# Performance work log

Measured on AMD Instinct MI355X. Metric: run time of the kernel, lower is better.

The kernel has to match this reference:

```python
import jax, jax.numpy as jnp
import numpy as np

B, N, D, E, F, K = 2, 2048, 768, 8, 3072, 2
V_MAX = 3.0
FEAT_CLAMP = 10.0


def setup_inputs() -> dict:
    key = jax.random.key(0)
    ks = jax.random.split(key, 8)
    s = lambda k, shape, sc: (jax.random.normal(k, shape, jnp.float32) * sc)
    return {
        "x": s(ks[0], (B, N, D), 1.0),
        "v_w": s(ks[1], (D,), 0.02),
        "v_b": jnp.zeros((), jnp.float32),
        "gate_w": s(ks[2], (D, E), 0.02),
        "gate_b": jnp.zeros((E,), jnp.float32),
        "w1": s(ks[3], (E, D, F), 0.02),
        "b1": jnp.zeros((E, F), jnp.float32),
        "w2": s(ks[4], (E, F, D), 0.02),
        "b2": jnp.zeros((E, D), jnp.float32),
        "out_w": s(ks[5], (2, D), 0.02),
        "out_b": jnp.zeros((D,), jnp.float32),
        "bk_scale": jnp.ones((D,), jnp.float32),
    }


def bk_green_diag(a):
    # a: (B, N) complex64 diagonal of (H_eps - z), unit off-diagonals.
    # Stable two-sided continued-fraction (Thomas/LDU) recursion:
    #   d_i = a_i - 1/d_{i-1},  e_i = a_i - 1/e_{i+1},  G_ii = 1/(d_i + e_i - a_i)
    aT = jnp.swapaxes(a, 0, 1)  # (N, B)

    def step(c, ai):
        d = ai - 1.0 / c
        return d, d

    d0 = aT[0]
    _, d_rest = jax.lax.scan(step, d0, aT[1:])
    d = jnp.concatenate([d0[None], d_rest], axis=0)  # (N, B)

    eN = aT[-1]
    _, e_rest = jax.lax.scan(step, eN, aT[:-1], reverse=True)
    e = jnp.concatenate([e_rest, eN[None]], axis=0)  # (N, B)

    G = 1.0 / (d + e - aT)
    return jnp.swapaxes(G, 0, 1)  # (B, N) complex


def reference(x, v_w, v_b, gate_w, gate_b, w1, b1, w2, b2, out_w, out_b, bk_scale):
    # --- potential projection: v = clamp(Linear(x), +-3) ---
    v = jnp.clip(x @ v_w + v_b, -V_MAX, V_MAX)  # (B, N)
    # H_eps diagonal = -2 + v, z = 1j  ->  A = H_eps - z
    a = ((-2.0 + v).astype(jnp.complex64) - 1j)
    G = bk_green_diag(a)  # (B, N) complex
    feats = jnp.stack([G.real, G.imag], axis=-1)  # (B, N, 2)

    # --- sparse MoE FFN (top-k softmax gating, GELU experts) ---
    logits = x @ gate_w + gate_b  # (B, N, E)
    probs = jax.nn.softmax(logits, axis=-1)
    topv, topi = jax.lax.top_k(probs, K)
    topv = topv / jnp.sum(topv, axis=-1, keepdims=True)
    comb = jnp.sum(topv[..., None] * jax.nn.one_hot(topi, E, dtype=x.dtype), axis=2)  # (B, N, E)
    h = jax.nn.gelu(jnp.einsum("bnd,edf->bnef", x, w1) + b1)  # (B, N, E, F)
    y = jnp.einsum("bnef,efd->bned", h, w2) + b2  # (B, N, E, D)
    ffn_out = jnp.einsum("bne,bned->bnd", comb, y)

    # --- spectral branch: clamp features, project to d_model, scale ---
    feats_c = jnp.clip(feats, -FEAT_CLAMP, FEAT_CLAMP)
    spec_out = feats_c @ out_w + out_b  # (B, N, D)
    return ffn_out + bk_scale * spec_out
```

## Files before the change

### kernel.cpp

```cpp
#include <hip/hip_runtime.h>
#include <hip/hip_bf16.h>

#define BB 2
#define NN 2048
#define DD 768
#define EE 8
#define FF 3072
#define TOK (BB*NN)
#define ROWS_CAP 9216
#define TILES 72

typedef __attribute__((ext_vector_type(8))) __bf16 bf16x8;
typedef __attribute__((ext_vector_type(4))) float floatx4;

#define OFF_CTRL    0ull
#define OFF_V       1024ull
#define OFF_TOKE    17408ull
#define OFF_TOKW    50176ull
#define OFF_ROWTOK  82944ull
#define OFF_ROWW    119808ull
#define OFF_SLOT    156672ull
#define OFF_FEATS   189440ull
#define OFF_W2T     222208ull
#define OFF_XBF     37970944ull
#define OFF_W1T     44262400ull
#define OFF_H       82011136ull
#define OFF_Y       OFF_XBF

__device__ __forceinline__ ushort f2b(float f) {
    union { float f; unsigned int i; } v; v.f = f;
    unsigned int u = v.i;
    unsigned int r = (u + 0x7FFFu + ((u >> 16) & 1u)) >> 16;
    return (ushort)r;
}
__device__ __forceinline__ unsigned int pk2(float lo, float hi) {
    union { float f; unsigned int u; } a, b;
    a.f = lo; b.f = hi;
    unsigned int ra = ((a.u + 0x7FFFu + ((a.u >> 16) & 1u)) >> 16) & 0xFFFFu;
    unsigned int rb = (b.u + 0x7FFFu + ((b.u >> 16) & 1u)) & 0xFFFF0000u;
    return ra | rb;
}
__device__ __forceinline__ float gelu_f(float x) {
    float z = 0.7978845608028654f * x * (1.f + 0.044715f * x * x);
    z = fminf(fmaxf(z, -12.f), 12.f);
    float e = __expf(2.f * z);
    return 0.5f * x * (1.f + (e - 1.f) / (e + 1.f));
}
__device__ __forceinline__ void gload16(const ushort* g, ushort* l) {
    __builtin_amdgcn_global_load_lds((const __attribute__((address_space(1))) void*)g,
                                     (__attribute__((address_space(3))) void*)l,
                                     16, 0, 0);
}

struct cplx { float x, y; };
__device__ __forceinline__ cplx cmulc(cplx a, cplx b) { return {a.x*b.x - a.y*b.y, a.x*b.y + a.y*b.x}; }
__device__ __forceinline__ cplx caddc(cplx a, cplx b) { return {a.x + b.x, a.y + b.y}; }
__device__ __forceinline__ cplx cdivc(cplx a, cplx b) {
    float s = 1.f / (b.x*b.x + b.y*b.y);
    return {(a.x*b.x + a.y*b.y)*s, (a.y*b.x - a.x*b.y)*s};
}
struct mob { cplx m00, m01, m10, m11; };
__device__ __forceinline__ mob mmul(const mob& A, const mob& B) {
    mob C;
    C.m00 = caddc(cmulc(A.m00, B.m00), cmulc(A.m01, B.m10));
    C.m01 = caddc(cmulc(A.m00, B.m01), cmulc(A.m01, B.m11));
    C.m10 = caddc(cmulc(A.m10, B.m00), cmulc(A.m11, B.m10));
    C.m11 = caddc(cmulc(A.m10, B.m01), cmulc(A.m11, B.m11));
    return C;
}
__device__ __forceinline__ void mnorm(mob& A) {
    float s = fabsf(A.m00.x);
    s = fmaxf(s, fabsf(A.m00.y)); s = fmaxf(s, fabsf(A.m01.x)); s = fmaxf(s, fabsf(A.m01.y));
    s = fmaxf(s, fabsf(A.m10.x)); s = fmaxf(s, fabsf(A.m10.y)); s = fmaxf(s, fabsf(A.m11.x));
    s = fmaxf(s, fabsf(A.m11.y));
    float r = 1.f / fmaxf(s, 1e-30f);
    A.m00.x *= r; A.m00.y *= r; A.m01.x *= r; A.m01.y *= r;
    A.m10.x *= r; A.m10.y *= r; A.m11.x *= r; A.m11.y *= r;
}
__device__ __forceinline__ mob mstep(cplx a, const mob& P) {
    mob C;
    C.m00 = {a.x*P.m00.x - a.y*P.m00.y - P.m10.x, a.x*P.m00.y + a.y*P.m00.x - P.m10.y};
    C.m01 = {a.x*P.m01.x - a.y*P.m01.y - P.m11.x, a.x*P.m01.y + a.y*P.m01.x - P.m11.y};
    C.m10 = P.m00; C.m11 = P.m01;
    return C;
}
__device__ __forceinline__ void mstore(float* s, const mob& A) {
    s[0]=A.m00.x; s[1]=A.m00.y; s[2]=A.m01.x; s[3]=A.m01.y;
    s[4]=A.m10.x; s[5]=A.m10.y; s[6]=A.m11.x; s[7]=A.m11.y;
}
__device__ __forceinline__ mob mload(const float* s) {
    mob A;
    A.m00 = {s[0], s[1]}; A.m01 = {s[2], s[3]};
    A.m10 = {s[4], s[5]}; A.m11 = {s[6], s[7]};
    return A;
}

#define NB_CVT   ((TOK*DD)/8/256)
#define NB_ROUTE (TOK/4)
#define NB_T1    ((FF/32)*(DD/32)*EE)
#define NB_T2    ((DD/32)*(FF/32)*EE)

__device__ __forceinline__ void cvt_body(const float* __restrict__ src, ushort* __restrict__ dst, int i) {
    const float4* s = ((const float4*)src) + (size_t)i * 2;
    float4 a = s[0], b = s[1];
    uint4 o;
    o.x = pk2(a.x, a.y); o.y = pk2(a.z, a.w);
    o.z = pk2(b.x, b.y); o.w = pk2(b.z, b.w);
    *(((uint4*)dst) + i) = o;
}

__device__ __forceinline__ void tcvt_body(const float* __restrict__ src, ushort* __restrict__ dst,
                                          int R, int C, int bx, int by, int bz,
                                          float (*t)[33]) {
    size_t eoff = (size_t)bz * R * C;
    const float* s = src + eoff;
    ushort* d = dst + eoff;
    int c0 = bx * 32, r0 = by * 32;
    int tid = threadIdx.x;
    int tr = tid >> 3, tc = (tid & 7) * 4;
    float4 vsrc = *(const float4*)(s + (size_t)(r0 + tr) * C + c0 + tc);
    t[tr][tc] = vsrc.x; t[tr][tc+1] = vsrc.y; t[tr][tc+2] = vsrc.z; t[tr][tc+3] = vsrc.w;
    __syncthreads();
    ushort4 o;
    o.x = f2b(t[tc  ][tr]);
    o.y = f2b(t[tc+1][tr]);
    o.z = f2b(t[tc+2][tr]);
    o.w = f2b(t[tc+3][tr]);
    *(ushort4*)(d + (size_t)(c0 + tr) * R + r0 + tc) = o;
}

__device__ __forceinline__ void routing_body(
    const float* __restrict__ x, const float* __restrict__ v_w, const float* __restrict__ v_b,
    const float* __restrict__ gate_w, const float* __restrict__ gate_b,
    float* __restrict__ v_out, int* __restrict__ tok_e, float* __restrict__ tok_w, int blk)
{
    int wave = threadIdx.x >> 6, lane = threadIdx.x & 63;
    int t = blk * 4 + wave;
    const float* xr = x + (size_t)t * DD;
    float av = 0.f;
    float ag[8] = {0.f, 0.f, 0.f, 0.f, 0.f, 0.f, 0.f, 0.f};
    #pragma unroll
    for (int i = 0; i < 12; i++) {
        int d = lane + 64 * i;
        float xv = xr[d];
        av += xv * v_w[d];
        const float4* g = (const float4*)(gate_w + d * 8);
        float4 g0 = g[0], g1 = g[1];
        ag[0] += xv * g0.x; ag[1] += xv * g0.y; ag[2] += xv * g0.z; ag[3] += xv * g0.w;
        ag[4] += xv * g1.x; ag[5] += xv * g1.y; ag[6] += xv * g1.z; ag[7] += xv * g1.w;
    }
    #pragma unroll
    for (int off = 32; off >= 1; off >>= 1) {
        av += __shfl_xor(av, off);
        #pragma unroll
        for (int e = 0; e < 8; e++) ag[e] += __shfl_xor(ag[e], off);
    }
    if (lane == 0) {
        float vv = av + v_b[0];
        vv = fminf(fmaxf(vv, -3.f), 3.f);
        v_out[t] = vv;
        float lg[8];
        #pragma unroll
        for (int e = 0; e < 8; e++) lg[e] = ag[e] + gate_b[e];
        int e0 = 0;
        #pragma unroll
        for (int e = 1; e < 8; e++) if (lg[e] > lg[e0]) e0 = e;
        int e1 = -1;
        #pragma unroll
        for (int e = 0; e < 8; e++) if (e != e0 && (e1 < 0 || lg[e] > lg[e1])) e1 = e;
        float w0 = 1.f / (1.f + __expf(lg[e1] - lg[e0]));
        tok_e[2*t] = e0; tok_e[2*t+1] = e1;
        tok_w[2*t] = w0; tok_w[2*t+1] = 1.f - w0;
    }
}

__global__ __launch_bounds__(256) void prep_kernel(
    const float* __restrict__ x, ushort* __restrict__ x_bf,
    const float* __restrict__ v_w, const float* __restrict__ v_b,
    const float* __restrict__ gate_w, const float* __restrict__ gate_b,
    float* __restrict__ v_out, int* __restrict__ tok_e, float* __restrict__ tok_w,
    const float* __restrict__ w1, ushort* __restrict__ w1t,
    const float* __restrict__ w2, ushort* __restrict__ w2t)
{
    __shared__ float t[32][33];
    int id = blockIdx.x;
    if (id < NB_CVT) {
        cvt_body(x, x_bf, id * 256 + threadIdx.x);
        return;
    }
    id -= NB_CVT;
    if (id < NB_ROUTE) {
        routing_body(x, v_w, v_b, gate_w, gate_b, v_out, tok_e, tok_w, id);
        return;
    }
    id -= NB_ROUTE;
    if (id < NB_T1) {
        int bx = id % (FF/32); int by = (id / (FF/32)) % (DD/32); int bz = id / ((FF/32)*(DD/32));
        tcvt_body(w1, w1t, DD, FF, bx, by, bz, t);
        return;
    }
    id -= NB_T1;
    {
        int bx = id % (DD/32); int by = (id / (DD/32)) % (FF/32); int bz = id / ((DD/32)*(FF/32));
        tcvt_body(w2, w2t, FF, DD, bx, by, bz, t);
    }
}

__device__ void setup_body(
    const int* __restrict__ tok_e, const float* __restrict__ tok_w,
    int* __restrict__ ctrl, int* __restrict__ row_token, float* __restrict__ row_w,
    int* __restrict__ slot)
{
    __shared__ int cnt[8], base[8], cursor[8];
    int tid = threadIdx.x;
    int lane = tid & 63;
    if (tid < 8) { cnt[tid] = 0; cursor[tid] = 0; }
    __syncthreads();

    int mye[8];
    #pragma unroll
    for (int it = 0; it < 8; it++) {
        int idx = it * 1024 + tid;
        int e = tok_e[idx];
        mye[it] = e;
        #pragma unroll
        for (int ex = 0; ex < 8; ex++) {
            unsigned long long m = __ballot(e == ex);
            if (e == ex && lane == (__ffsll((long long)m) - 1))
                atomicAdd(&cnt[ex], (int)__popcll(m));
        }
    }
    __syncthreads();
    if (tid == 0) {
        int b = 0;
        int* te = ctrl + 24;
        for (int i = 0; i < TILES; i++) te[i] = -1;
        #pragma unroll
        for (int e = 0; e < EE; e++) {
            base[e] = b;
            ctrl[16 + e] = b;
            int tiles = (cnt[e] + 127) >> 7;
            int t0 = b >> 7;
            for (int i = 0; i < tiles; i++) te[t0 + i] = e;
            b += tiles << 7;
        }
    }
    for (int p = tid; p < ROWS_CAP; p += 1024) row_token[p] = -1;
    __syncthreads();

    #pragma unroll
    for (int it = 0; it < 8; it++) {
        int idx = it * 1024 + tid;
        int e = mye[it];
        unsigned long long lt = (1ull << lane) - 1ull;
        int p = 0;
        #pragma unroll
        for (int ex = 0; ex < 8; ex++) {
            unsigned long long m = __ballot(e == ex);
            if (e == ex) {
                int leader = __ffsll((long long)m) - 1;
                int pos = (int)__popcll(m & lt);
                int bp = 0;
                if (lane == leader) bp = atomicAdd(&cursor[ex], (int)__popcll(m));
                bp = __shfl(bp, leader);
                p = base[ex] + bp + pos;
            }
        }
        row_token[p] = idx >> 1;
        row_w[p] = tok_w[idx];
        slot[idx] = p;
    }
}

__device__ void bk_body(int b, const float* __restrict__ v, float* __restrict__ feats) {
    int t = threadIdx.x;
    bool act = t < 256;
    __shared__ float sm[256][8];
    const mob I = {{1.f,0.f},{0.f,0.f},{0.f,0.f},{1.f,0.f}};
    cplx a[8];
    const float* vb = v + (size_t)b * NN;
    if (act) {
        #pragma unroll
        for (int j = 0; j < 8; j++) { a[j].x = -2.f + vb[t*8 + j]; a[j].y = -1.f; }
    }

    mob cur = I;
    if (act) {
        #pragma unroll
        for (int j = 0; j < 8; j++) cur = mstep(a[j], cur);
        mnorm(cur);
        mstore(sm[t], cur);
    }
    for (int s = 1; s < 256; s <<= 1) {
        __syncthreads();
        mob prev; bool has = act && (t >= s);
        if (has) prev = mload(sm[t - s]);
        __syncthreads();
        if (has) { cur = mmul(cur, prev); mnorm(cur); mstore(sm[t], cur); }
    }
    __syncthreads();
    cplx dreg[8];
    if (act) {
        mob P = (t > 0) ? mload(sm[t - 1]) : I;
        #pragma unroll
        for (int j = 0; j < 8; j++) {
            P = mstep(a[j], P); mnorm(P);
            dreg[j] = cdivc(P.m00, P.m10);
        }
    }
    __syncthreads();

    cur = I;
    if (act) {
        #pragma unroll
        for (int j = 7; j >= 0; j--) cur = mstep(a[j], cur);
        mnorm(cur);
        mstore(sm[t], cur);
    }
    for (int s = 1; s < 256; s <<= 1) {
        __syncthreads();
        mob nxt; bool has = act && (t + s < 256);
        if (has) nxt = mload(sm[t + s]);
        __syncthreads();
        if (has) { cur = mmul(cur, nxt); mnorm(cur); mstore(sm[t], cur); }
    }
    __syncthreads();
    if (act) {
        mob P = (t < 255) ? mload(sm[t + 1]) : I;
        #pragma unroll
        for (int j = 7; j >= 0; j--) {
            P = mstep(a[j], P); mnorm(P);
            cplx e = cdivc(P.m00, P.m10);
            cplx den = {dreg[j].x + e.x - a[j].x, dreg[j].y + e.y - a[j].y};
            cplx one = {1.f, 0.f};
            cplx G = cdivc(one, den);
            int i = b * NN + t*8 + j;
            feats[2*i]   = G.x;
            feats[2*i+1] = G.y;
        }
    }
}

__global__ __launch_bounds__(1024) void setup_bk_kernel(
    const int* __restrict__ tok_e, const float* __restrict__ tok_w,
    int* __restrict__ ctrl, int* __restrict__ row_token, float* __restrict__ row_w,
    int* __restrict__ slot, const float* __restrict__ v, float* __restrict__ feats)
{
    if (blockIdx.x == 0) setup_body(tok_e, tok_w, ctrl, row_token, row_w, slot);
    else                 bk_body(blockIdx.x - 1, v, feats);
}

#define STAGE64(AW, BW, k0) do { \
        _Pragma("unroll") \
        for (int g = 0; g < 4; g++) { \
            gload16(ag[g] + (k0), (AW) + g*8*64); \
            gload16(bg[g] + (k0), (BW) + g*8*64); \
        } } while (0)

#define LOADFR64(APTR, BPTR, QX) do { \
        _Pragma("unroll") \
        for (int i = 0; i < 4; i++) \
            afr[i] = *(const bf16x8*)(const void*)((APTR) + (wm + i*16 + lm) * 64 + (QX)); \
        _Pragma("unroll") \
        for (int j = 0; j < 4; j++) \
            bfr[j] = *(const bf16x8*)(const void*)((BPTR) + (wn + j*16 + lm) * 64 + (QX)); \
    } while (0)

#define MFMAS() do { \
        _Pragma("unroll") \
        for (int i = 0; i < 4; i++) \
            _Pragma("unroll") \
            for (int j = 0; j < 4; j++) \
                acc[i][j] = __builtin_amdgcn_mfma_f32_16x16x32_bf16(afr[i], bfr[j], acc[i][j], 0, 0, 0); \
    } while (0)

#define PIPE64(NK) do { \
    STAGE64(AsW0, BsW0, 0); \
    STAGE64(AsW1, BsW1, 64); \
    for (int ks = 0; ks < (NK); ks++) { \
        int cur = ks & 1; \
        const ushort* Ab = cur ? As[1] : As[0]; \
        const ushort* Bb = cur ? Bs[1] : Bs[0]; \
        ushort* AsN = cur ? AsW1 : AsW0; \
        ushort* BsN = cur ? BsW1 : BsW0; \
        if (ks < (NK) - 1) { asm volatile("s_waitcnt vmcnt(8)" ::: "memory"); } \
        else               { asm volatile("s_waitcnt vmcnt(0)" ::: "memory"); } \
        __builtin_amdgcn_s_barrier(); \
        { \
            bf16x8 afr[4], bfr[4]; \
            LOADFR64(Ab, Bb, qx0); \
            __builtin_amdgcn_s_setprio(1); \
            MFMAS(); \
            __builtin_amdgcn_s_setprio(0); \
        } \
        { \
            bf16x8 afr[4], bfr[4]; \
            LOADFR64(Ab, Bb, qx0 ^ 32); \
            asm volatile("s_waitcnt lgkmcnt(0)" ::: "memory"); \
            __builtin_amdgcn_sched_barrier(0); \
            __builtin_amdgcn_s_barrier(); \
            if (ks + 2 < (NK)) STAGE64(AsN, BsN, ks*64 + 128); \
            __builtin_amdgcn_s_setprio(1); \
            MFMAS(); \
            __builtin_amdgcn_s_setprio(0); \
        } \
    } } while (0)

__global__ __launch_bounds__(256) void gemm1_kernel(
    const ushort* __restrict__ x_bf, const ushort* __restrict__ w1t, const float* __restrict__ b1,
    const int* __restrict__ ctrl, const int* __restrict__ row_token, ushort* __restrict__ H)
{
    int tile = blockIdx.y;
    int e = ctrl[24 + tile];
    if (e < 0) return;
    int p0 = tile * 128;
    int f0 = blockIdx.x * 128;

    __shared__ ushort As[2][128 * 64];
    __shared__ ushort Bs[2][128 * 64];
    __shared__ int toks[128];

    int tid = threadIdx.x;
    if (tid < 128) { int tk = row_token[p0 + tid]; toks[tid] = tk < 0 ? 0 : tk; }
    __syncthreads();

    int wave = tid >> 6, lane = tid & 63;
    int srow = lane >> 3;
    int kq = (((lane & 7) ^ (srow & 7))) * 8;
    const ushort* ag[4];
    #pragma unroll
    for (int g = 0; g < 4; g++) {
        int tk = toks[wave*32 + g*8 + srow];
        ag[g] = x_bf + (size_t)tk * DD + kq;
    }
    const ushort* w1e = w1t + (size_t)e * (FF * DD);
    const ushort* bg[4];
    #pragma unroll
    for (int g = 0; g < 4; g++)
        bg[g] = w1e + (size_t)(f0 + wave*32 + g*8 + srow) * DD + kq;
    ushort* AsW0 = &As[0][wave * 32 * 64];
    ushort* BsW0 = &Bs[0][wave * 32 * 64];
    ushort* AsW1 = &As[1][wave * 32 * 64];
    ushort* BsW1 = &Bs[1][wave * 32 * 64];

    floatx4 zero4 = {0.f, 0.f, 0.f, 0.f};
    floatx4 acc[4][4];
    #pragma unroll
    for (int i = 0; i < 4; i++)
        #pragma unroll
        for (int j = 0; j < 4; j++) acc[i][j] = zero4;

    int wm = (wave & 1) * 64, wn = (wave >> 1) * 64;
    int lm = lane & 15, q = lane >> 4;
    int qx0 = (q ^ (lm & 7)) * 8;

    PIPE64(DD/64);

    #pragma unroll
    for (int i = 0; i < 4; i++) {
        #pragma unroll
        for (int j = 0; j < 4; j++) {
            int n = wn + j*16 + lm;
            float bias = b1[e * FF + f0 + n];
            #pragma unroll
            for (int r = 0; r < 4; r++) {
                int m = wm + i*16 + q*4 + r;
                float hv = gelu_f(acc[i][j][r] + bias);
                H[(size_t)(p0 + m) * FF + f0 + n] = f2b(hv);
            }
        }
    }
}

__global__ __launch_bounds__(256) void gemm2_kernel(
    const ushort* __restrict__ H, const ushort* __restrict__ w2t, const float* __restrict__ b2,
    const int* __restrict__ ctrl, const float* __restrict__ row_w, float* __restrict__ Y)
{
    int tile = blockIdx.x;
    int e = ctrl[24 + tile];
    if (e < 0) return;
    int p0 = tile * 128;
    int d0 = blockIdx.y * 128;

    __shared__ ushort As[2][128 * 64];
    __shared__ ushort Bs[2][128 * 64];

    int tid = threadIdx.x;
    int wave = tid >> 6, lane = tid & 63;
    int srow = lane >> 3;
    int kq = (((lane & 7) ^ (srow & 7))) * 8;
    const ushort* ag[4];
    #pragma unroll
    for (int g = 0; g < 4; g++)
        ag[g] = H + (size_t)(p0 + wave*32 + g*8 + srow) * FF + kq;
    const ushort* w2e = w2t + (size_t)e * (DD * FF);
    const ushort* bg[4];
    #pragma unroll
    for (int g = 0; g < 4; g++)
        bg[g] = w2e + (size_t)(d0 + wave*32 + g*8 + srow) * FF + kq;
    ushort* AsW0 = &As[0][wave * 32 * 64];
    ushort* BsW0 = &Bs[0][wave * 32 * 64];
    ushort* AsW1 = &As[1][wave * 32 * 64];
    ushort* BsW1 = &Bs[1][wave * 32 * 64];

    floatx4 zero4 = {0.f, 0.f, 0.f, 0.f};
    floatx4 acc[4][4];
    #pragma unroll
    for (int i = 0; i < 4; i++)
        #pragma unroll
        for (int j = 0; j < 4; j++) acc[i][j] = zero4;

    int wm = (wave & 1) * 64, wn = (wave >> 1) * 64;
    int lm = lane & 15, q = lane >> 4;
    int qx0 = (q ^ (lm & 7)) * 8;

    PIPE64(FF/64);

    #pragma unroll
    for (int i = 0; i < 4; i++) {
        #pragma unroll
        for (int j = 0; j < 4; j++) {
            int n = wn + j*16 + lm;
            float bias = b2[e * DD + d0 + n];
            #pragma unroll
            for (int r = 0; r < 4; r++) {
                int m = wm + i*16 + q*4 + r;
                float wgt = row_w[p0 + m];
                Y[(size_t)(p0 + m) * DD + d0 + n] = wgt * (acc[i][j][r] + bias);
            }
        }
    }
}

__global__ __launch_bounds__(256) void final_kernel(
    const float* __restrict__ Y, const int* __restrict__ slot, const float* __restrict__ feats,
    const float* __restrict__ out_w, const float* __restrict__ out_b,
    const float* __restrict__ bk_scale, float* __restrict__ out)
{
    int idx = blockIdx.x * 256 + threadIdx.x;
    int base = idx * 4;
    int t = base / DD;
    int d = base - t * DD;
    int p0 = slot[2*t], p1 = slot[2*t + 1];
    const float4 ya = *(const float4*)(Y + (size_t)p0 * DD + d);
    const float4 yb = *(const float4*)(Y + (size_t)p1 * DD + d);
    float f0 = feats[2*t], f1 = feats[2*t + 1];
    f0 = fminf(fmaxf(f0, -10.f), 10.f);
    f1 = fminf(fmaxf(f1, -10.f), 10.f);
    float ff[4] = {ya.x + yb.x, ya.y + yb.y, ya.z + yb.z, ya.w + yb.w};
    float4 o;
    float* op = (float*)&o;
    #pragma unroll
    for (int u = 0; u < 4; u++) {
        float spec = f0 * out_w[d + u] + f1 * out_w[DD + d + u] + out_b[d + u];
        op[u] = ff[u] + bk_scale[d + u] * spec;
    }
    *(float4*)(out + base) = o;
}

extern "C" void kernel_launch(void* const* d_in, const int* in_sizes, int n_in,
                              void* d_out, int out_size, void* d_ws, size_t ws_size,
                              hipStream_t stream)
{
    const float* x      = (const float*)d_in[0];
    const float* v_w    = (const float*)d_in[1];
    const float* v_b    = (const float*)d_in[2];
    const float* gate_w = (const float*)d_in[3];
    const float* gate_b = (const float*)d_in[4];
    const float* w1     = (const float*)d_in[5];
    const float* b1     = (const float*)d_in[6];
    const float* w2     = (const float*)d_in[7];
    const float* b2     = (const float*)d_in[8];
    const float* out_w  = (const float*)d_in[9];
    const float* out_b  = (const float*)d_in[10];
    const float* bk_s   = (const float*)d_in[11];

    char* ws = (char*)d_ws;
    int*    ctrl    = (int*)(ws + OFF_CTRL);
    float*  v       = (float*)(ws + OFF_V);
    int*    tok_e   = (int*)(ws + OFF_TOKE);
    float*  tok_w   = (float*)(ws + OFF_TOKW);
    int*    row_tok = (int*)(ws + OFF_ROWTOK);
    float*  row_w   = (float*)(ws + OFF_ROWW);
    int*    slot    = (int*)(ws + OFF_SLOT);
    float*  feats   = (float*)(ws + OFF_FEATS);
    ushort* w2t     = (ushort*)(ws + OFF_W2T);
    ushort* x_bf    = (ushort*)(ws + OFF_XBF);
    ushort* w1t     = (ushort*)(ws + OFF_W1T);
    ushort* H       = (ushort*)(ws + OFF_H);
    float*  Y       = (float*)(ws + OFF_Y);
    float*  out     = (float*)d_out;

    prep_kernel<<<NB_CVT + NB_ROUTE + NB_T1 + NB_T2, 256, 0, stream>>>(
        x, x_bf, v_w, v_b, gate_w, gate_b, v, tok_e, tok_w, w1, w1t, w2, w2t);
    setup_bk_kernel<<<1 + BB, 1024, 0, stream>>>(tok_e, tok_w, ctrl, row_tok, row_w, slot, v, feats);
    gemm1_kernel<<<dim3(FF / 128, TILES), 256, 0, stream>>>(x_bf, w1t, b1, ctrl, row_tok, H);
    gemm2_kernel<<<dim3(TILES, DD / 128), 256, 0, stream>>>(H, w2t, b2, ctrl, row_w, Y);
    final_kernel<<<(TOK * DD) / 1024, 256, 0, stream>>>(Y, slot, feats, out_w, out_b, bk_s, out);
}
```

Before: 209.9 us.

## Restructure gemm1 into 512-thread blocks covering two row tiles with K=32 stages

The grouped GEMM1 now runs 512-thread blocks that each handle two consecutive 128-row tiles, which may belong to different experts. Each half uses its own expert's weight slice, and the K dimension is staged in steps of 32 instead of 64, using a new swizzle and a deeper effective pipeline. The weight-transpose conversion blocks also each process four 32x32 tiles, which cuts the number of blocks fourfold. The goal is better occupancy and fewer launched blocks and barriers per output, at the cost of more K iterations. It also relies on the ctrl expert layout matching the two-tile pairing.

```diff
diff --git a/kernel.cpp b/kernel.cpp
--- a/kernel.cpp
+++ b/kernel.cpp
@@ -97,8 +97,8 @@
 
 #define NB_CVT   ((TOK*DD)/8/256)
 #define NB_ROUTE (TOK/4)
-#define NB_T1    ((FF/32)*(DD/32)*EE)
-#define NB_T2    ((DD/32)*(FF/32)*EE)
+#define NB_T1    ((FF/128)*(DD/32)*EE)
+#define NB_T2    ((DD/128)*(FF/32)*EE)
 
 __device__ __forceinline__ void cvt_body(const float* __restrict__ src, ushort* __restrict__ dst, int i) {
     const float4* s = ((const float4*)src) + (size_t)i * 2;
@@ -109,24 +109,31 @@
     *(((uint4*)dst) + i) = o;
 }
 
-__device__ __forceinline__ void tcvt_body(const float* __restrict__ src, ushort* __restrict__ dst,
-                                          int R, int C, int bx, int by, int bz,
-                                          float (*t)[33]) {
+__device__ __forceinline__ void tcvt4_body(const float* __restrict__ src, ushort* __restrict__ dst,
+                                           int R, int C, int bx, int by, int bz,
+                                           float (*t)[33]) {
     size_t eoff = (size_t)bz * R * C;
     const float* s = src + eoff;
     ushort* d = dst + eoff;
-    int c0 = bx * 32, r0 = by * 32;
+    int c0 = bx * 128, r0 = by * 32;
     int tid = threadIdx.x;
     int tr = tid >> 3, tc = (tid & 7) * 4;
-    float4 vsrc = *(const float4*)(s + (size_t)(r0 + tr) * C + c0 + tc);
-    t[tr][tc] = vsrc.x; t[tr][tc+1] = vsrc.y; t[tr][tc+2] = vsrc.z; t[tr][tc+3] = vsrc.w;
-    __syncthreads();
-    ushort4 o;
-    o.x = f2b(t[tc  ][tr]);
-    o.y = f2b(t[tc+1][tr]);
-    o.z = f2b(t[tc+2][tr]);
-    o.w = f2b(t[tc+3][tr]);
-    *(ushort4*)(d + (size_t)(c0 + tr) * R + r0 + tc) = o;
+    float4 v[4];
+    const float* srow = s + (size_t)(r0 + tr) * C + c0 + tc;
+    #pragma unroll
+    for (int k = 0; k < 4; k++) v[k] = *(const float4*)(srow + k * 32);
+    #pragma unroll
+    for (int k = 0; k < 4; k++) {
+        __syncthreads();
+        t[tr][tc] = v[k].x; t[tr][tc+1] = v[k].y; t[tr][tc+2] = v[k].z; t[tr][tc+3] = v[k].w;
+        __syncthreads();
+        ushort4 o;
+        o.x = f2b(t[tc  ][tr]);
+        o.y = f2b(t[tc+1][tr]);
+        o.z = f2b(t[tc+2][tr]);
+        o.w = f2b(t[tc+3][tr]);
+        *(ushort4*)(d + (size_t)(c0 + k*32 + tr) * R + r0 + tc) = o;
+    }
 }
 
 __device__ __forceinline__ void routing_body(
@@ -195,14 +202,14 @@
     }
     id -= NB_ROUTE;
     if (id < NB_T1) {
-        int bx = id % (FF/32); int by = (id / (FF/32)) % (DD/32); int bz = id / ((FF/32)*(DD/32));
-        tcvt_body(w1, w1t, DD, FF, bx, by, bz, t);
+        int bx = id % (FF/128); int by = (id / (FF/128)) % (DD/32); int bz = id / ((FF/128)*(DD/32));
+        tcvt4_body(w1, w1t, DD, FF, bx, by, bz, t);
         return;
     }
     id -= NB_T1;
     {
-        int bx = id % (DD/32); int by = (id / (DD/32)) % (FF/32); int bz = id / ((DD/32)*(FF/32));
-        tcvt_body(w2, w2t, FF, DD, bx, by, bz, t);
+        int bx = id % (DD/128); int by = (id / (DD/128)) % (FF/32); int bz = id / ((DD/128)*(FF/32));
+        tcvt4_body(w2, w2t, FF, DD, bx, by, bz, t);
     }
 }
 
@@ -350,6 +357,113 @@
     else                 bk_body(blockIdx.x - 1, v, feats);
 }
 
+#define MFMAS() do { \
+        _Pragma("unroll") \
+        for (int i = 0; i < 4; i++) \
+            _Pragma("unroll") \
+            for (int j = 0; j < 4; j++) \
+                acc[i][j] = __builtin_amdgcn_mfma_f32_16x16x32_bf16(afr[i], bfr[j], acc[i][j], 0, 0, 0); \
+    } while (0)
+
+__global__ __launch_bounds__(512, 4) void gemm1_kernel(
+    const ushort* __restrict__ x_bf, const ushort* __restrict__ w1t, const float* __restrict__ b1,
+    const int* __restrict__ ctrl, const int* __restrict__ row_token, ushort* __restrict__ H)
+{
+    int tile = blockIdx.y;
+    int e0 = ctrl[24 + 2*tile];
+    if (e0 < 0) return;
+    int e1 = ctrl[24 + 2*tile + 1];
+    if (e1 < 0) e1 = e0;
+    int p0 = tile * 256;
+    int f0 = blockIdx.x * 128;
+
+    __shared__ ushort As[2][256 * 32];
+    __shared__ ushort Bs[2][256 * 32];
+    __shared__ int toks[256];
+
+    int tid = threadIdx.x;
+    if (tid < 256) { int tk = row_token[p0 + tid]; toks[tid] = tk < 0 ? 0 : tk; }
+    __syncthreads();
+
+    int wave = tid >> 6, lane = tid & 63;
+    int rsub = lane >> 2;
+    int kq = (((lane & 3) ^ ((rsub >> 1) & 3))) * 8;
+    int tokA0 = toks[wave*32 + rsub];
+    int tokA1 = toks[wave*32 + 16 + rsub];
+    const ushort* aglob0 = x_bf + (size_t)tokA0 * DD + kq;
+    const ushort* aglob1 = x_bf + (size_t)tokA1 * DD + kq;
+    int eh = (wave >> 2) ? e1 : e0;
+    const ushort* w1e = w1t + (size_t)eh * (FF * DD);
+    const ushort* bglob0 = w1e + (size_t)(f0 + (wave & 3)*32 + rsub) * DD + kq;
+    const ushort* bglob1 = bglob0 + (size_t)16 * DD;
+    ushort* AsW0 = &As[0][wave * 32 * 32];
+    ushort* BsW0 = &Bs[0][wave * 32 * 32];
+    ushort* AsW1 = &As[1][wave * 32 * 32];
+    ushort* BsW1 = &Bs[1][wave * 32 * 32];
+
+    floatx4 zero4 = {0.f, 0.f, 0.f, 0.f};
+    floatx4 acc[4][4];
+    #pragma unroll
+    for (int i = 0; i < 4; i++)
+        #pragma unroll
+        for (int j = 0; j < 4; j++) acc[i][j] = zero4;
+
+    int wm = (wave >> 1) * 64, wn = (wave & 1) * 64;
+    int bbase = (wave >> 2) * 128;
+    int lm = lane & 15, q = lane >> 4;
+    int qx = (q ^ ((lm >> 1) & 3)) * 8;
+
+    #define G1_STAGE(AW, BW, k0) do { \
+        gload16(aglob0 + (k0), (AW)); \
+        gload16(aglob1 + (k0), (AW) + 16*32); \
+        gload16(bglob0 + (k0), (BW)); \
+        gload16(bglob1 + (k0), (BW) + 16*32); } while (0)
+
+    G1_STAGE(AsW0, BsW0, 0);
+    G1_STAGE(AsW1, BsW1, 32);
+    const int NK = DD / 32;
+    for (int ks = 0; ks < NK; ks++) {
+        int cur = ks & 1;
+        const ushort* Ab = cur ? As[1] : As[0];
+        const ushort* Bb = cur ? Bs[1] : Bs[0];
+        ushort* AsN = cur ? AsW1 : AsW0;
+        ushort* BsN = cur ? BsW1 : BsW0;
+        if (ks < NK - 1) { asm volatile("s_waitcnt vmcnt(4)" ::: "memory"); }
+        else             { asm volatile("s_waitcnt vmcnt(0)" ::: "memory"); }
+        __builtin_amdgcn_s_barrier();
+        bf16x8 afr[4], bfr[4];
+        #pragma unroll
+        for (int i = 0; i < 4; i++)
+            afr[i] = *(const bf16x8*)(const void*)(Ab + (wm + i*16 + lm) * 32 + qx);
+        #pragma unroll
+        for (int j = 0; j < 4; j++)
+            bfr[j] = *(const bf16x8*)(const void*)(Bb + (bbase + wn + j*16 + lm) * 32 + qx);
+        asm volatile("s_waitcnt lgkmcnt(0)" ::: "memory");
+        __builtin_amdgcn_sched_barrier(0);
+        __builtin_amdgcn_s_barrier();
+        if (ks + 2 < NK) G1_STAGE(AsN, BsN, ks*32 + 64);
+        __builtin_amdgcn_s_setprio(1);
+        MFMAS();
+        __builtin_amdgcn_s_setprio(0);
+    }
+    #undef G1_STAGE
+
+    #pragma unroll
+    for (int i = 0; i < 4; i++) {
+        #pragma unroll
+        for (int j = 0; j < 4; j++) {
+            int n = wn + j*16 + lm;
+            float bias = b1[eh * FF + f0 + n];
+            #pragma unroll
+            for (int r = 0; r < 4; r++) {
+                int m = wm + i*16 + q*4 + r;
+                float hv = gelu_f(acc[i][j][r] + bias);
+                H[(size_t)(p0 + m) * FF + f0 + n] = f2b(hv);
+            }
+        }
+    }
+}
+
 #define STAGE64(AW, BW, k0) do { \
         _Pragma("unroll") \
         for (int g = 0; g < 4; g++) { \
@@ -364,14 +478,6 @@
         _Pragma("unroll") \
         for (int j = 0; j < 4; j++) \
             bfr[j] = *(const bf16x8*)(const void*)((BPTR) + (wn + j*16 + lm) * 64 + (QX)); \
-    } while (0)
-
-#define MFMAS() do { \
-        _Pragma("unroll") \
-        for (int i = 0; i < 4; i++) \
-            _Pragma("unroll") \
-            for (int j = 0; j < 4; j++) \
-                acc[i][j] = __builtin_amdgcn_mfma_f32_16x16x32_bf16(afr[i], bfr[j], acc[i][j], 0, 0, 0); \
     } while (0)
 
 #define PIPE64(NK) do { \
@@ -406,72 +512,6 @@
         } \
     } } while (0)
 
-__global__ __launch_bounds__(256) void gemm1_kernel(
-    const ushort* __restrict__ x_bf, const ushort* __restrict__ w1t, const float* __restrict__ b1,
-    const int* __restrict__ ctrl, const int* __restrict__ row_token, ushort* __restrict__ H)
-{
-    int tile = blockIdx.y;
-    int e = ctrl[24 + tile];
-    if (e < 0) return;
-    int p0 = tile * 128;
-    int f0 = blockIdx.x * 128;
-
-    __shared__ ushort As[2][128 * 64];
-    __shared__ ushort Bs[2][128 * 64];
-    __shared__ int toks[128];
-
-    int tid = threadIdx.x;
-    if (tid < 128) { int tk = row_token[p0 + tid]; toks[tid] = tk < 0 ? 0 : tk; }
-    __syncthreads();
-
-    int wave = tid >> 6, lane = tid & 63;
-    int srow = lane >> 3;
-    int kq = (((lane & 7) ^ (srow & 7))) * 8;
-    const ushort* ag[4];
-    #pragma unroll
-    for (int g = 0; g < 4; g++) {
-        int tk = toks[wave*32 + g*8 + srow];
-        ag[g] = x_bf + (size_t)tk * DD + kq;
-    }
-    const ushort* w1e = w1t + (size_t)e * (FF * DD);
-    const ushort* bg[4];
-    #pragma unroll
-    for (int g = 0; g < 4; g++)
-        bg[g] = w1e + (size_t)(f0 + wave*32 + g*8 + srow) * DD + kq;
-    ushort* AsW0 = &As[0][wave * 32 * 64];
-    ushort* BsW0 = &Bs[0][wave * 32 * 64];
-    ushort* AsW1 = &As[1][wave * 32 * 64];
-    ushort* BsW1 = &Bs[1][wave * 32 * 64];
-
-    floatx4 zero4 = {0.f, 0.f, 0.f, 0.f};
-    floatx4 acc[4][4];
-    #pragma unroll
-    for (int i = 0; i < 4; i++)
-        #pragma unroll
-        for (int j = 0; j < 4; j++) acc[i][j] = zero4;
-
-    int wm = (wave & 1) * 64, wn = (wave >> 1) * 64;
-    int lm = lane & 15, q = lane >> 4;
-    int qx0 = (q ^ (lm & 7)) * 8;
-
-    PIPE64(DD/64);
-
-    #pragma unroll
-    for (int i = 0; i < 4; i++) {
-        #pragma unroll
-        for (int j = 0; j < 4; j++) {
-            int n = wn + j*16 + lm;
-            float bias = b1[e * FF + f0 + n];
-            #pragma unroll
-            for (int r = 0; r < 4; r++) {
-                int m = wm + i*16 + q*4 + r;
-                float hv = gelu_f(acc[i][j][r] + bias);
-                H[(size_t)(p0 + m) * FF + f0 + n] = f2b(hv);
-            }
-        }
-    }
-}
-
 __global__ __launch_bounds__(256) void gemm2_kernel(
     const ushort* __restrict__ H, const ushort* __restrict__ w2t, const float* __restrict__ b2,
     const int* __restrict__ ctrl, const float* __restrict__ row_w, float* __restrict__ Y)
@@ -594,7 +634,7 @@
     prep_kernel<<<NB_CVT + NB_ROUTE + NB_T1 + NB_T2, 256, 0, stream>>>(
         x, x_bf, v_w, v_b, gate_w, gate_b, v, tok_e, tok_w, w1, w1t, w2, w2t);
     setup_bk_kernel<<<1 + BB, 1024, 0, stream>>>(tok_e, tok_w, ctrl, row_tok, row_w, slot, v, feats);
-    gemm1_kernel<<<dim3(FF / 128, TILES), 256, 0, stream>>>(x_bf, w1t, b1, ctrl, row_tok, H);
+    gemm1_kernel<<<dim3(FF / 128, TILES / 2), 512, 0, stream>>>(x_bf, w1t, b1, ctrl, row_tok, H);
     gemm2_kernel<<<dim3(TILES, DD / 128), 256, 0, stream>>>(H, w2t, b2, ctrl, row_w, Y);
     final_kernel<<<(TOK * DD) / 1024, 256, 0, stream>>>(Y, slot, feats, out_w, out_b, bk_s, out);
 }
```

Measured after the change: 208.4 us (median of 2 runs). Within noise of the previous version (-0.7%).
